# Kernel optimization log

Hardware: AMD Instinct MI355X
Metric: run time of the kernel (lower is better)

## Reference

```python
import jax, jax.numpy as jnp
import numpy as np
import math


def _omega_np(nrows: int, ncols: int, rng: np.random.RandomState) -> np.ndarray:
    # Block-orthogonal random feature matrix, transposed to (ncols, nrows)
    nblocks = int(nrows / ncols)
    blocks = []
    for _ in range(nblocks):
        q, _ = np.linalg.qr(rng.normal(size=(ncols, ncols)))
        blocks.append(q.T)
    missing = nrows - nblocks * ncols
    if missing > 0:
        q, _ = np.linalg.qr(rng.normal(size=(ncols, ncols)))
        blocks.append(q.T[:missing])
    norm = np.linalg.norm(rng.normal(size=(nrows, ncols)), axis=1, keepdims=True)
    return (norm * np.vstack(blocks)).T  # (ncols, nrows) = (dim_qk, m)


def setup_inputs() -> dict:
    N, DIM_QK, DIM_V, M = 262144, 128, 128, 256
    key = jax.random.key(0)
    kq, kk, kv = jax.random.split(key, 3)
    Q = jax.random.normal(kq, (N, DIM_QK), dtype=jnp.float32)
    K = jax.random.normal(kk, (N, DIM_QK), dtype=jnp.float32)
    V = jax.random.normal(kv, (N, DIM_V), dtype=jnp.float32)
    omega = jnp.asarray(_omega_np(M, DIM_QK, np.random.RandomState(0)), dtype=jnp.float32)
    return {"Q": Q, "K": K, "V": V, "omega": omega}


def _phi(X, omega, is_query: bool, eps: float = 1e-4):
    d = X.shape[-1]
    m = omega.shape[-1]
    U = jnp.matmul(X / d ** 0.25, omega)                       # [N, m]
    h = jnp.sum(X * X, axis=-1, keepdims=True) / (2.0 * d ** 0.5)
    if is_query:
        maximum = jnp.max(U, axis=-1, keepdims=True)
    else:
        maximum = jnp.max(U)
    return (jnp.exp(U - h - maximum) + eps) / math.sqrt(m)


def reference(Q, K, V, omega):
    eps = 1e-8
    Qp = _phi(Q, omega, True)    # [N, m]
    Kp = _phi(K, omega, False)   # [N, m]
    norm = Qp @ jnp.sum(Kp, axis=0) + eps                       # [N]
    # Faithful to einsum('nF,nF,nf->nf', Qp, Kp, V): row-wise dot * V
    w = jnp.sum(Qp * Kp, axis=-1, keepdims=True)                # [N, 1]
    return w * V / norm[:, None]                                # [N, dim_v]
```

## Files before the change

kernel.cpp:

```cpp
#include <hip/hip_runtime.h>
#include <hip/hip_bf16.h>


typedef _Float16 f16x8 __attribute__((ext_vector_type(8)));
typedef float f32x4 __attribute__((ext_vector_type(4)));

#define D_QK 128
#define M_F  256
#define OMT_HALVES 32768

constexpr float D4      = 0.29730177875068026f;
constexpr float H_SCALE = 0.044194173824159216f;

__device__ __forceinline__ unsigned f2key(float f) {
  unsigned b = __float_as_uint(f);
  return (b & 0x80000000u) ? ~b : (b | 0x80000000u);
}
__device__ __forceinline__ float key2f(unsigned k) {
  return (k & 0x80000000u) ? __uint_as_float(k & 0x7fffffffu) : __uint_as_float(~k);
}

__device__ __forceinline__ f32x4 mfma16(f16x8 a, f16x8 b, f32x4 c) {
  return __builtin_amdgcn_mfma_f32_16x16x32_f16(a, b, c, 0, 0, 0);
}

__device__ __forceinline__ void load_frag(const float* __restrict__ row, int ks, int q,
                                          f16x8& a, float& h) {
  const float4* p = (const float4*)(row + ks * 32 + q * 8);
  float4 x0 = p[0], x1 = p[1];
  h += x0.x*x0.x + x0.y*x0.y + x0.z*x0.z + x0.w*x0.w
     + x1.x*x1.x + x1.y*x1.y + x1.z*x1.z + x1.w*x1.w;
  a[0] = (_Float16)(x0.x * D4); a[1] = (_Float16)(x0.y * D4);
  a[2] = (_Float16)(x0.z * D4); a[3] = (_Float16)(x0.w * D4);
  a[4] = (_Float16)(x1.x * D4); a[5] = (_Float16)(x1.y * D4);
  a[6] = (_Float16)(x1.z * D4); a[7] = (_Float16)(x1.w * D4);
}

__device__ __forceinline__ f16x8 bfrag(const _Float16* om_lds, int t, int ks, int lane) {
  return *(const f16x8*)&om_lds[(((t << 2) | ks) << 9) + (lane << 3)];
}

extern "C" __global__ void k_prep(const float* __restrict__ om, _Float16* __restrict__ omt,
                                  float* __restrict__ S, unsigned* __restrict__ Mkey) {
  int i = blockIdx.x * 256 + threadIdx.x;
  if (i < OMT_HALVES) {
    int t = i >> 11, ks = (i >> 9) & 3, l = (i >> 3) & 63, j = i & 7;
    int d = ks * 32 + ((l >> 4) << 3) + j;
    int m = t * 16 + (l & 15);
    omt[i] = (_Float16)om[d * M_F + m];
  }
  if (blockIdx.x == 0) {
    S[threadIdx.x] = 0.f;
    if (threadIdx.x == 0) *Mkey = 0u;
  }
}

__global__ __launch_bounds__(256, 2) void k_kstats(
    const float* __restrict__ K, const _Float16* __restrict__ omt,
    float* __restrict__ Lout, float* __restrict__ Pout, unsigned* __restrict__ Mkey) {
  __shared__ __align__(16) _Float16 om_lds[OMT_HALVES];
  __shared__ float P_lds[4][256];
  __shared__ float red_lds[4];
  int tid = threadIdx.x;
  int w = tid >> 6, lane = tid & 63, q = lane >> 4, c = lane & 15;
  int rb = blockIdx.x * 64 + w * 16;

  const float4* osrc = (const float4*)omt;
  float4 st[16];
#pragma unroll
  for (int i = 0; i < 16; ++i) st[i] = osrc[tid + i * 256];

  const float* krow = K + (size_t)(rb + c) * D_QK;
  f16x8 ak[4];
  float hk = 0.f;
#pragma unroll
  for (int ks = 0; ks < 4; ++ks) load_frag(krow, ks, q, ak[ks], hk);
  hk += __shfl_xor(hk, 16, 64);
  hk += __shfl_xor(hk, 32, 64);
  hk *= H_SCALE;

  float4* odst = (float4*)om_lds;
#pragma unroll
  for (int i = 0; i < 16; ++i) odst[tid + i * 256] = st[i];

  const f32x4 zero = {0.f, 0.f, 0.f, 0.f};
  f32x4 cc[16];
#pragma unroll
  for (int t = 0; t < 16; ++t) cc[t] = zero;
  __syncthreads();

#pragma unroll
  for (int t = 0; t < 16; ++t) {
#pragma unroll
    for (int ks = 0; ks < 4; ++ks) {
      f16x8 b = bfrag(om_lds, t, ks, lane);
      cc[t] = mfma16(ak[ks], b, cc[t]);
    }
  }

  float mx = cc[0][0];
#pragma unroll
  for (int t = 0; t < 16; ++t)
    mx = fmaxf(mx, fmaxf(fmaxf(cc[t][0], cc[t][1]), fmaxf(cc[t][2], cc[t][3])));
#pragma unroll
  for (int m = 1; m <= 32; m <<= 1) mx = fmaxf(mx, __shfl_xor(mx, m, 64));
  if (lane == 0) red_lds[w] = mx;
  __syncthreads();
  float Lb = fmaxf(fmaxf(red_lds[0], red_lds[1]), fmaxf(red_lds[2], red_lds[3]));

  float hr[4];
#pragma unroll
  for (int r = 0; r < 4; ++r) hr[r] = __shfl(hk, q * 4 + r, 64);

#pragma unroll
  for (int t = 0; t < 16; ++t) {
    float s = __expf(cc[t][0] - hr[0] - Lb) + __expf(cc[t][1] - hr[1] - Lb)
            + __expf(cc[t][2] - hr[2] - Lb) + __expf(cc[t][3] - hr[3] - Lb);
    s += __shfl_xor(s, 16, 64);
    s += __shfl_xor(s, 32, 64);
    if (q == 0) P_lds[w][t * 16 + c] = s;
  }
  __syncthreads();
  Pout[(size_t)blockIdx.x * 256 + tid] =
      P_lds[0][tid] + P_lds[1][tid] + P_lds[2][tid] + P_lds[3][tid];
  if (tid == 0) {
    Lout[blockIdx.x] = Lb;
    atomicMax(Mkey, f2key(Lb));
  }
}

extern "C" __global__ void k_combine(const float* __restrict__ Lout, const float* __restrict__ Pout,
                                     const unsigned* __restrict__ Mkey, float* __restrict__ Mout,
                                     float* __restrict__ S) {
  float M = key2f(*Mkey);
  if (blockIdx.x == 0 && threadIdx.x == 0) *Mout = M;
  int b0 = blockIdx.x * 8;
  float acc = 0.f;
#pragma unroll
  for (int i = 0; i < 8; ++i) {
    int b = b0 + i;
    float f = __expf(Lout[b] - M);
    acc += f * Pout[(size_t)b * 256 + threadIdx.x];
  }
  atomicAdd(&S[threadIdx.x], acc);
}

__global__ __launch_bounds__(256, 2) void k_main(
    const float* __restrict__ Q, const float* __restrict__ K, const float* __restrict__ V,
    const _Float16* __restrict__ omt, const float* __restrict__ Sws,
    const float* __restrict__ Mws, float* __restrict__ out, float epsN) {
  __shared__ __align__(16) _Float16 om_lds[OMT_HALVES];
  __shared__ float S_lds[256];
  __shared__ float scale_lds[64];
  int tid = threadIdx.x;
  int w = tid >> 6, lane = tid & 63, q = lane >> 4, c = lane & 15;
  int rb = blockIdx.x * 64 + w * 16;

  const float4* osrc = (const float4*)omt;
  float4 st[16];
#pragma unroll
  for (int i = 0; i < 16; ++i) st[i] = osrc[tid + i * 256];

  S_lds[tid] = (Sws[tid] + epsN) * 0.0625f;
  float Mglob = *Mws;

  const float* qrow = Q + (size_t)(rb + c) * D_QK;
  const float* krow = K + (size_t)(rb + c) * D_QK;
  f16x8 aq[4], ak[4];
  float hq = 0.f, hk = 0.f;
#pragma unroll
  for (int ks = 0; ks < 4; ++ks) {
    load_frag(qrow, ks, q, aq[ks], hq);
    load_frag(krow, ks, q, ak[ks], hk);
  }
  hq += __shfl_xor(hq, 16, 64); hq += __shfl_xor(hq, 32, 64); hq *= H_SCALE;
  hk += __shfl_xor(hk, 16, 64); hk += __shfl_xor(hk, 32, 64); hk *= H_SCALE;

  float4* odst = (float4*)om_lds;
#pragma unroll
  for (int i = 0; i < 16; ++i) odst[tid + i * 256] = st[i];

  const f32x4 zero = {0.f, 0.f, 0.f, 0.f};
  f32x4 cq[16], ck[16];
#pragma unroll
  for (int t = 0; t < 16; ++t) { cq[t] = zero; ck[t] = zero; }
  __syncthreads();

#pragma unroll
  for (int t = 0; t < 16; ++t) {
#pragma unroll
    for (int ks = 0; ks < 4; ++ks) {
      f16x8 b = bfrag(om_lds, t, ks, lane);
      cq[t] = mfma16(aq[ks], b, cq[t]);
      ck[t] = mfma16(ak[ks], b, ck[t]);
    }
  }

  float hqr[4], hkr[4];
#pragma unroll
  for (int r = 0; r < 4; ++r) {
    hqr[r] = __shfl(hq, q * 4 + r, 64);
    hkr[r] = __shfl(hk, q * 4 + r, 64);
  }

#pragma unroll
  for (int r = 0; r < 4; ++r) {
    float mx = cq[0][r];
#pragma unroll
    for (int t = 1; t < 16; ++t) mx = fmaxf(mx, cq[t][r]);
#pragma unroll
    for (int m = 1; m <= 8; m <<= 1) mx = fmaxf(mx, __shfl_xor(mx, m, 64));
    float wsum = 0.f, nsum = 0.f;
#pragma unroll
    for (int t = 0; t < 16; ++t) {
      float qp = __expf(cq[t][r] - hqr[r] - mx) + 1e-4f;
      float kp = __expf(ck[t][r] - hkr[r] - Mglob) + 1e-4f;
      wsum += qp * kp;
      nsum += qp * S_lds[t * 16 + c];
    }
#pragma unroll
    for (int m = 1; m <= 8; m <<= 1) {
      wsum += __shfl_xor(wsum, m, 64);
      nsum += __shfl_xor(nsum, m, 64);
    }
    if (c == 0)
      scale_lds[w * 16 + q * 4 + r] = (wsum * (1.f / 256.f)) / (nsum * 0.0625f + 1e-8f);
  }
  __syncthreads();

  const float4* vsrc = (const float4*)(V + (size_t)blockIdx.x * 64 * D_QK);
  float4* odst4 = (float4*)(out + (size_t)blockIdx.x * 64 * D_QK);
#pragma unroll
  for (int i = 0; i < 8; ++i) {
    int j = tid + i * 256;
    float s = scale_lds[j >> 5];
    float4 v = vsrc[j];
    odst4[j] = make_float4(v.x * s, v.y * s, v.z * s, v.w * s);
  }
}

extern "C" void kernel_launch(void* const* d_in, const int* in_sizes, int n_in,
                              void* d_out, int out_size, void* d_ws, size_t ws_size,
                              hipStream_t stream) {
  const float* Q  = (const float*)d_in[0];
  const float* K  = (const float*)d_in[1];
  const float* V  = (const float*)d_in[2];
  const float* om = (const float*)d_in[3];
  float* out = (float*)d_out;
  int N = in_sizes[0] / D_QK;
  int nblk = N / 64;

  char* ws = (char*)d_ws;
  _Float16* omt = (_Float16*)ws;
  size_t off = (size_t)OMT_HALVES * 2;
  float* Lout = (float*)(ws + off);   off += (size_t)nblk * 4;
  float* Pout = (float*)(ws + off);   off += (size_t)nblk * 256 * 4;
  float* S    = (float*)(ws + off);   off += 1024;
  unsigned* Mkey = (unsigned*)(ws + off); off += 16;
  float* Mout = (float*)(ws + off);

  hipLaunchKernelGGL(k_prep, dim3((OMT_HALVES + 255) / 256), dim3(256), 0, stream,
                     om, omt, S, Mkey);
  hipLaunchKernelGGL(k_kstats, dim3(nblk), dim3(256), 0, stream, K, omt, Lout, Pout, Mkey);
  hipLaunchKernelGGL(k_combine, dim3(nblk / 8), dim3(256), 0, stream, Lout, Pout, Mkey, Mout, S);
  hipLaunchKernelGGL(k_main, dim3(nblk), dim3(256), 0, stream, Q, K, V, omt, S, Mout, out,
                     (float)N * 1e-4f);
}
```

Baseline: 450.2 us.

## Make stats and main kernels persistent with prefetch and per-wave online max

Both the K-statistics and main kernels now launch a fixed grid of 512 blocks that loop over several 64-row tiles. This amortises the 64KB omega LDS load per block and prefetches the next tile's Q/K rows into registers while the current tile's MFMAs run. k_kstats now keeps a per-wave running max with rescaled partial sums (online softmax style) and drops its block-level syncs. k_main scales V per wave through shuffles instead of an LDS scale buffer and a barrier. The costs are lower grid parallelism (512 blocks over 256 CUs) and more register pressure from the prefetch buffers.

```diff
diff --git a/kernel.cpp b/kernel.cpp
--- a/kernel.cpp
+++ b/kernel.cpp
@@ -8,6 +8,7 @@
 #define D_QK 128
 #define M_F  256
 #define OMT_HALVES 32768
+#define GBLK 512
 
 constexpr float D4      = 0.29730177875068026f;
 constexpr float H_SCALE = 0.044194173824159216f;
@@ -24,10 +25,8 @@
   return __builtin_amdgcn_mfma_f32_16x16x32_f16(a, b, c, 0, 0, 0);
 }
 
-__device__ __forceinline__ void load_frag(const float* __restrict__ row, int ks, int q,
+__device__ __forceinline__ void conv_frag(const float4& x0, const float4& x1,
                                           f16x8& a, float& h) {
-  const float4* p = (const float4*)(row + ks * 32 + q * 8);
-  float4 x0 = p[0], x1 = p[1];
   h += x0.x*x0.x + x0.y*x0.y + x0.z*x0.z + x0.w*x0.w
      + x1.x*x1.x + x1.y*x1.y + x1.z*x1.z + x1.w*x1.w;
   a[0] = (_Float16)(x0.x * D4); a[1] = (_Float16)(x0.y * D4);
@@ -57,75 +56,96 @@
 
 __global__ __launch_bounds__(256, 2) void k_kstats(
     const float* __restrict__ K, const _Float16* __restrict__ omt,
-    float* __restrict__ Lout, float* __restrict__ Pout, unsigned* __restrict__ Mkey) {
+    float* __restrict__ Lout, float* __restrict__ Pout, unsigned* __restrict__ Mkey,
+    int T) {
   __shared__ __align__(16) _Float16 om_lds[OMT_HALVES];
-  __shared__ float P_lds[4][256];
-  __shared__ float red_lds[4];
   int tid = threadIdx.x;
   int w = tid >> 6, lane = tid & 63, q = lane >> 4, c = lane & 15;
-  int rb = blockIdx.x * 64 + w * 16;
 
   const float4* osrc = (const float4*)omt;
-  float4 st[16];
-#pragma unroll
-  for (int i = 0; i < 16; ++i) st[i] = osrc[tid + i * 256];
-
-  const float* krow = K + (size_t)(rb + c) * D_QK;
-  f16x8 ak[4];
-  float hk = 0.f;
-#pragma unroll
-  for (int ks = 0; ks < 4; ++ks) load_frag(krow, ks, q, ak[ks], hk);
-  hk += __shfl_xor(hk, 16, 64);
-  hk += __shfl_xor(hk, 32, 64);
-  hk *= H_SCALE;
-
   float4* odst = (float4*)om_lds;
 #pragma unroll
-  for (int i = 0; i < 16; ++i) odst[tid + i * 256] = st[i];
-
-  const f32x4 zero = {0.f, 0.f, 0.f, 0.f};
-  f32x4 cc[16];
-#pragma unroll
-  for (int t = 0; t < 16; ++t) cc[t] = zero;
+  for (int i = 0; i < 16; ++i) odst[tid + i * 256] = osrc[tid + i * 256];
+
+  size_t row0 = (size_t)blockIdx.x * T * 64 + w * 16 + c;
+  const float4* kptr = (const float4*)(K + row0 * D_QK) + q * 2;
+
+  float4 kf[8];
+#pragma unroll
+  for (int ks = 0; ks < 4; ++ks) {
+    kf[ks * 2] = kptr[ks * 8]; kf[ks * 2 + 1] = kptr[ks * 8 + 1];
+  }
+
+  float Pw[16];
+#pragma unroll
+  for (int t = 0; t < 16; ++t) Pw[t] = 0.f;
+  float Lrun = -1e30f;
+
   __syncthreads();
 
-#pragma unroll
-  for (int t = 0; t < 16; ++t) {
-#pragma unroll
-    for (int ks = 0; ks < 4; ++ks) {
-      f16x8 b = bfrag(om_lds, t, ks, lane);
-      cc[t] = mfma16(ak[ks], b, cc[t]);
-    }
-  }
-
-  float mx = cc[0][0];
-#pragma unroll
-  for (int t = 0; t < 16; ++t)
-    mx = fmaxf(mx, fmaxf(fmaxf(cc[t][0], cc[t][1]), fmaxf(cc[t][2], cc[t][3])));
-#pragma unroll
-  for (int m = 1; m <= 32; m <<= 1) mx = fmaxf(mx, __shfl_xor(mx, m, 64));
-  if (lane == 0) red_lds[w] = mx;
-  __syncthreads();
-  float Lb = fmaxf(fmaxf(red_lds[0], red_lds[1]), fmaxf(red_lds[2], red_lds[3]));
-
-  float hr[4];
-#pragma unroll
-  for (int r = 0; r < 4; ++r) hr[r] = __shfl(hk, q * 4 + r, 64);
-
-#pragma unroll
-  for (int t = 0; t < 16; ++t) {
-    float s = __expf(cc[t][0] - hr[0] - Lb) + __expf(cc[t][1] - hr[1] - Lb)
-            + __expf(cc[t][2] - hr[2] - Lb) + __expf(cc[t][3] - hr[3] - Lb);
-    s += __shfl_xor(s, 16, 64);
-    s += __shfl_xor(s, 32, 64);
-    if (q == 0) P_lds[w][t * 16 + c] = s;
-  }
-  __syncthreads();
-  Pout[(size_t)blockIdx.x * 256 + tid] =
-      P_lds[0][tid] + P_lds[1][tid] + P_lds[2][tid] + P_lds[3][tid];
-  if (tid == 0) {
-    Lout[blockIdx.x] = Lb;
-    atomicMax(Mkey, f2key(Lb));
+  for (int it = 0; it < T; ++it) {
+    f16x8 ak[4];
+    float hk = 0.f;
+#pragma unroll
+    for (int ks = 0; ks < 4; ++ks) conv_frag(kf[ks * 2], kf[ks * 2 + 1], ak[ks], hk);
+    hk += __shfl_xor(hk, 16, 64);
+    hk += __shfl_xor(hk, 32, 64);
+    hk *= H_SCALE;
+
+    kptr += 2048;
+    if (it + 1 < T) {
+#pragma unroll
+      for (int ks = 0; ks < 4; ++ks) {
+        kf[ks * 2] = kptr[ks * 8]; kf[ks * 2 + 1] = kptr[ks * 8 + 1];
+      }
+    }
+
+    const f32x4 zero = {0.f, 0.f, 0.f, 0.f};
+    f32x4 cc[16];
+#pragma unroll
+    for (int t = 0; t < 16; ++t) cc[t] = zero;
+#pragma unroll
+    for (int t = 0; t < 16; ++t) {
+#pragma unroll
+      for (int ks = 0; ks < 4; ++ks) {
+        f16x8 b = bfrag(om_lds, t, ks, lane);
+        cc[t] = mfma16(ak[ks], b, cc[t]);
+      }
+    }
+
+    float hr[4];
+#pragma unroll
+    for (int r = 0; r < 4; ++r) hr[r] = __shfl(hk, q * 4 + r, 64);
+
+    float mx = cc[0][0];
+#pragma unroll
+    for (int t = 0; t < 16; ++t)
+      mx = fmaxf(mx, fmaxf(fmaxf(cc[t][0], cc[t][1]), fmaxf(cc[t][2], cc[t][3])));
+#pragma unroll
+    for (int m = 1; m <= 32; m <<= 1) mx = fmaxf(mx, __shfl_xor(mx, m, 64));
+
+    float newL = fmaxf(Lrun, mx);
+    float fr = __expf(Lrun - newL);
+
+#pragma unroll
+    for (int t = 0; t < 16; ++t) {
+      float s = __expf(cc[t][0] - hr[0] - newL) + __expf(cc[t][1] - hr[1] - newL)
+              + __expf(cc[t][2] - hr[2] - newL) + __expf(cc[t][3] - hr[3] - newL);
+      s += __shfl_xor(s, 16, 64);
+      s += __shfl_xor(s, 32, 64);
+      Pw[t] = Pw[t] * fr + s;
+    }
+    Lrun = newL;
+  }
+
+  int wid = blockIdx.x * 4 + w;
+  if (q == 0) {
+#pragma unroll
+    for (int t = 0; t < 16; ++t) Pout[(size_t)wid * 256 + t * 16 + c] = Pw[t];
+  }
+  if (lane == 0) {
+    Lout[wid] = Lrun;
+    atomicMax(Mkey, f2key(Lrun));
   }
 }
 
@@ -134,13 +154,12 @@
                                      float* __restrict__ S) {
   float M = key2f(*Mkey);
   if (blockIdx.x == 0 && threadIdx.x == 0) *Mout = M;
-  int b0 = blockIdx.x * 8;
+  int g0 = blockIdx.x * 32;
   float acc = 0.f;
 #pragma unroll
-  for (int i = 0; i < 8; ++i) {
-    int b = b0 + i;
-    float f = __expf(Lout[b] - M);
-    acc += f * Pout[(size_t)b * 256 + threadIdx.x];
+  for (int i = 0; i < 32; ++i) {
+    int g = g0 + i;
+    acc += __expf(Lout[g] - M) * Pout[(size_t)g * 256 + threadIdx.x];
   }
   atomicAdd(&S[threadIdx.x], acc);
 }
@@ -148,94 +167,111 @@
 __global__ __launch_bounds__(256, 2) void k_main(
     const float* __restrict__ Q, const float* __restrict__ K, const float* __restrict__ V,
     const _Float16* __restrict__ omt, const float* __restrict__ Sws,
-    const float* __restrict__ Mws, float* __restrict__ out, float epsN) {
+    const float* __restrict__ Mws, float* __restrict__ out, float epsN, int T) {
   __shared__ __align__(16) _Float16 om_lds[OMT_HALVES];
   __shared__ float S_lds[256];
-  __shared__ float scale_lds[64];
   int tid = threadIdx.x;
   int w = tid >> 6, lane = tid & 63, q = lane >> 4, c = lane & 15;
-  int rb = blockIdx.x * 64 + w * 16;
 
   const float4* osrc = (const float4*)omt;
-  float4 st[16];
-#pragma unroll
-  for (int i = 0; i < 16; ++i) st[i] = osrc[tid + i * 256];
-
+  float4* odst = (float4*)om_lds;
+#pragma unroll
+  for (int i = 0; i < 16; ++i) odst[tid + i * 256] = osrc[tid + i * 256];
   S_lds[tid] = (Sws[tid] + epsN) * 0.0625f;
   float Mglob = *Mws;
 
-  const float* qrow = Q + (size_t)(rb + c) * D_QK;
-  const float* krow = K + (size_t)(rb + c) * D_QK;
-  f16x8 aq[4], ak[4];
-  float hq = 0.f, hk = 0.f;
+  size_t row0 = (size_t)blockIdx.x * T * 64 + w * 16 + c;
+  const float4* qptr = (const float4*)(Q + row0 * D_QK) + q * 2;
+  const float4* kptr = (const float4*)(K + row0 * D_QK) + q * 2;
+
+  float4 qf[8], kf[8];
 #pragma unroll
   for (int ks = 0; ks < 4; ++ks) {
-    load_frag(qrow, ks, q, aq[ks], hq);
-    load_frag(krow, ks, q, ak[ks], hk);
-  }
-  hq += __shfl_xor(hq, 16, 64); hq += __shfl_xor(hq, 32, 64); hq *= H_SCALE;
-  hk += __shfl_xor(hk, 16, 64); hk += __shfl_xor(hk, 32, 64); hk *= H_SCALE;
-
-  float4* odst = (float4*)om_lds;
-#pragma unroll
-  for (int i = 0; i < 16; ++i) odst[tid + i * 256] = st[i];
-
-  const f32x4 zero = {0.f, 0.f, 0.f, 0.f};
-  f32x4 cq[16], ck[16];
-#pragma unroll
-  for (int t = 0; t < 16; ++t) { cq[t] = zero; ck[t] = zero; }
+    qf[ks * 2] = qptr[ks * 8]; qf[ks * 2 + 1] = qptr[ks * 8 + 1];
+    kf[ks * 2] = kptr[ks * 8]; kf[ks * 2 + 1] = kptr[ks * 8 + 1];
+  }
   __syncthreads();
 
-#pragma unroll
-  for (int t = 0; t < 16; ++t) {
+  for (int it = 0; it < T; ++it) {
+    f16x8 aq[4], ak[4];
+    float hq = 0.f, hk = 0.f;
 #pragma unroll
     for (int ks = 0; ks < 4; ++ks) {
-      f16x8 b = bfrag(om_lds, t, ks, lane);
-      cq[t] = mfma16(aq[ks], b, cq[t]);
-      ck[t] = mfma16(ak[ks], b, ck[t]);
-    }
-  }
-
-  float hqr[4], hkr[4];
-#pragma unroll
-  for (int r = 0; r < 4; ++r) {
-    hqr[r] = __shfl(hq, q * 4 + r, 64);
-    hkr[r] = __shfl(hk, q * 4 + r, 64);
-  }
-
-#pragma unroll
-  for (int r = 0; r < 4; ++r) {
-    float mx = cq[0][r];
-#pragma unroll
-    for (int t = 1; t < 16; ++t) mx = fmaxf(mx, cq[t][r]);
-#pragma unroll
-    for (int m = 1; m <= 8; m <<= 1) mx = fmaxf(mx, __shfl_xor(mx, m, 64));
-    float wsum = 0.f, nsum = 0.f;
+      conv_frag(qf[ks * 2], qf[ks * 2 + 1], aq[ks], hq);
+      conv_frag(kf[ks * 2], kf[ks * 2 + 1], ak[ks], hk);
+    }
+    hq += __shfl_xor(hq, 16, 64); hq += __shfl_xor(hq, 32, 64); hq *= H_SCALE;
+    hk += __shfl_xor(hk, 16, 64); hk += __shfl_xor(hk, 32, 64); hk *= H_SCALE;
+
+    qptr += 2048; kptr += 2048;
+    if (it + 1 < T) {
+#pragma unroll
+      for (int ks = 0; ks < 4; ++ks) {
+        qf[ks * 2] = qptr[ks * 8]; qf[ks * 2 + 1] = qptr[ks * 8 + 1];
+        kf[ks * 2] = kptr[ks * 8]; kf[ks * 2 + 1] = kptr[ks * 8 + 1];
+      }
+    }
+
+    const f32x4 zero = {0.f, 0.f, 0.f, 0.f};
+    f32x4 cq[16], ck[16];
+#pragma unroll
+    for (int t = 0; t < 16; ++t) { cq[t] = zero; ck[t] = zero; }
 #pragma unroll
     for (int t = 0; t < 16; ++t) {
-      float qp = __expf(cq[t][r] - hqr[r] - mx) + 1e-4f;
-      float kp = __expf(ck[t][r] - hkr[r] - Mglob) + 1e-4f;
-      wsum += qp * kp;
-      nsum += qp * S_lds[t * 16 + c];
-    }
-#pragma unroll
-    for (int m = 1; m <= 8; m <<= 1) {
-      wsum += __shfl_xor(wsum, m, 64);
-      nsum += __shfl_xor(nsum, m, 64);
-    }
-    if (c == 0)
-      scale_lds[w * 16 + q * 4 + r] = (wsum * (1.f / 256.f)) / (nsum * 0.0625f + 1e-8f);
-  }
-  __syncthreads();
-
-  const float4* vsrc = (const float4*)(V + (size_t)blockIdx.x * 64 * D_QK);
-  float4* odst4 = (float4*)(out + (size_t)blockIdx.x * 64 * D_QK);
-#pragma unroll
-  for (int i = 0; i < 8; ++i) {
-    int j = tid + i * 256;
-    float s = scale_lds[j >> 5];
-    float4 v = vsrc[j];
-    odst4[j] = make_float4(v.x * s, v.y * s, v.z * s, v.w * s);
+#pragma unroll
+      for (int ks = 0; ks < 4; ++ks) {
+        f16x8 b = bfrag(om_lds, t, ks, lane);
+        cq[t] = mfma16(aq[ks], b, cq[t]);
+        ck[t] = mfma16(ak[ks], b, ck[t]);
+      }
+    }
+
+    size_t f4base = ((size_t)blockIdx.x * T + it) * 2048 + (size_t)w * 512;
+    const float4* vp = (const float4*)V + f4base;
+    float4 vf[8];
+#pragma unroll
+    for (int i = 0; i < 8; ++i) vf[i] = vp[i * 64 + lane];
+
+    float hqr[4], hkr[4];
+#pragma unroll
+    for (int r = 0; r < 4; ++r) {
+      hqr[r] = __shfl(hq, q * 4 + r, 64);
+      hkr[r] = __shfl(hk, q * 4 + r, 64);
+    }
+
+    float sc[4];
+#pragma unroll
+    for (int r = 0; r < 4; ++r) {
+      float mx = cq[0][r];
+#pragma unroll
+      for (int t = 1; t < 16; ++t) mx = fmaxf(mx, cq[t][r]);
+#pragma unroll
+      for (int m = 1; m <= 8; m <<= 1) mx = fmaxf(mx, __shfl_xor(mx, m, 64));
+      float wsum = 0.f, nsum = 0.f;
+#pragma unroll
+      for (int t = 0; t < 16; ++t) {
+        float qp = __expf(cq[t][r] - hqr[r] - mx) + 1e-4f;
+        float kp = __expf(ck[t][r] - hkr[r] - Mglob) + 1e-4f;
+        wsum += qp * kp;
+        nsum += qp * S_lds[t * 16 + c];
+      }
+#pragma unroll
+      for (int m = 1; m <= 8; m <<= 1) {
+        wsum += __shfl_xor(wsum, m, 64);
+        nsum += __shfl_xor(nsum, m, 64);
+      }
+      sc[r] = (wsum * (1.f / 256.f)) / (nsum * 0.0625f + 1e-8f);
+    }
+
+    float4* op = (float4*)out + f4base;
+#pragma unroll
+    for (int i = 0; i < 8; ++i) {
+      float s_lo = __shfl(sc[(2 * i) & 3], ((2 * i) >> 2) << 4, 64);
+      float s_hi = __shfl(sc[(2 * i + 1) & 3], ((2 * i + 1) >> 2) << 4, 64);
+      float s = (lane < 32) ? s_lo : s_hi;
+      float4 v = vf[i];
+      op[i * 64 + lane] = make_float4(v.x * s, v.y * s, v.z * s, v.w * s);
+    }
   }
 }
 
@@ -249,20 +285,22 @@
   float* out = (float*)d_out;
   int N = in_sizes[0] / D_QK;
   int nblk = N / 64;
+  int T = nblk / GBLK;
+  int NG = GBLK * 4;
 
   char* ws = (char*)d_ws;
   _Float16* omt = (_Float16*)ws;
   size_t off = (size_t)OMT_HALVES * 2;
-  float* Lout = (float*)(ws + off);   off += (size_t)nblk * 4;
-  float* Pout = (float*)(ws + off);   off += (size_t)nblk * 256 * 4;
+  float* Lout = (float*)(ws + off);   off += (size_t)NG * 4;
+  float* Pout = (float*)(ws + off);   off += (size_t)NG * 256 * 4;
   float* S    = (float*)(ws + off);   off += 1024;
   unsigned* Mkey = (unsigned*)(ws + off); off += 16;
   float* Mout = (float*)(ws + off);
 
   hipLaunchKernelGGL(k_prep, dim3((OMT_HALVES + 255) / 256), dim3(256), 0, stream,
                      om, omt, S, Mkey);
-  hipLaunchKernelGGL(k_kstats, dim3(nblk), dim3(256), 0, stream, K, omt, Lout, Pout, Mkey);
-  hipLaunchKernelGGL(k_combine, dim3(nblk / 8), dim3(256), 0, stream, Lout, Pout, Mkey, Mout, S);
-  hipLaunchKernelGGL(k_main, dim3(nblk), dim3(256), 0, stream, Q, K, V, omt, S, Mout, out,
-                     (float)N * 1e-4f);
-}
+  hipLaunchKernelGGL(k_kstats, dim3(GBLK), dim3(256), 0, stream, K, omt, Lout, Pout, Mkey, T);
+  hipLaunchKernelGGL(k_combine, dim3(NG / 32), dim3(256), 0, stream, Lout, Pout, Mkey, Mout, S);
+  hipLaunchKernelGGL(k_main, dim3(GBLK), dim3(256), 0, stream, Q, K, V, omt, S, Mout, out,
+                     (float)N * 1e-4f, T);
+}
```

New measurement: 815.9 us. 1.81x slower.
